# Kernel optimization log

Hardware: AMD Instinct MI355X
Metric: run time of the kernel (lower is better)

Reference implementation:

```python
import jax, jax.numpy as jnp
import numpy as np

LN_EPS = 1e-5
DIM = 128
HEADS = 6
DIM_HEAD = 32
INNER = HEADS * DIM_HEAD          # 192
FF_INNER = int(DIM * 4 * 2 / 3)   # 341 (GEGLU inner dim)
LOCAL_WINDOW = 200
CACHE = 3
COMPRESS = 2
TW = LOCAL_WINDOW + CACHE         # 203
B = 2
T = 12800                         # 32 chunks of 400


def layer_norm(x, w, b):
    m = x.mean(-1, keepdims=True)
    v = ((x - m) ** 2).mean(-1, keepdims=True)
    return (x - m) / jnp.sqrt(v + LN_EPS) * w + b


def apply_rotary(q, k):
    # q, k: (b, h, n, d); standard half-rotation rotary over absolute positions
    d = q.shape[-1]
    n = q.shape[2]
    inv_freq = 1.0 / (10000.0 ** (jnp.arange(0, d, 2, dtype=jnp.float32) / d))
    freqs = jnp.arange(n, dtype=jnp.float32)[:, None] * inv_freq  # (n, d/2)
    emb = jnp.concatenate([freqs, freqs], axis=-1)                # (n, d)
    cos = jnp.cos(emb).astype(q.dtype)
    sin = jnp.sin(emb).astype(q.dtype)

    def rot_half(x):
        x1, x2 = jnp.split(x, 2, axis=-1)
        return jnp.concatenate([-x2, x1], axis=-1)

    rope = lambda x: x * cos + rot_half(x) * sin
    return rope(q), rope(k)


def local_attention(q, k, v, w):
    # causal local attention, look_backward=1 window, look_forward=0 (lucidrains LocalAttention)
    b, h, n, d = q.shape
    nw = n // w
    q, k = apply_rotary(q, k)
    qw = q.reshape(b, h, nw, w, d)

    def look_around(x):
        xw = x.reshape(b, h, nw, w, d)
        prev = jnp.pad(xw[:, :, :-1], ((0, 0), (0, 0), (1, 0), (0, 0), (0, 0)))
        return jnp.concatenate([prev, xw], axis=3)  # (b,h,nw,2w,d)

    kw = look_around(k)
    vw = look_around(v)

    t = jnp.arange(n).reshape(nw, w)
    tk_prev = jnp.pad(t[:-1], ((1, 0), (0, 0)), constant_values=-1)
    tk = jnp.concatenate([tk_prev, t], axis=1)  # (nw, 2w); -1 marks padding
    mask = (t[:, :, None] >= tk[:, None, :]) & (tk[:, None, :] >= 0)  # (nw, w, 2w)

    sim = jnp.einsum('bhwid,bhwjd->bhwij', qw, kw) * (d ** -0.5)
    neg = jnp.finfo(sim.dtype).min
    sim = jnp.where(mask[None, None], sim, neg)
    attn = jax.nn.softmax(sim, axis=-1)
    out = jnp.einsum('bhwij,bhwjd->bhwid', attn, vw)
    return out.reshape(b, h, n, d)


def local_mha(x, ln_w, ln_b, wqkv, wo, window):
    h = layer_norm(x, ln_w, ln_b)
    qkv = h @ wqkv                       # (b, n, 3*INNER)
    q, k, v = jnp.split(qkv, 3, axis=-1)

    def split_heads(t):
        bb, n, _ = t.shape
        return t.reshape(bb, n, HEADS, DIM_HEAD).transpose(0, 2, 1, 3)

    out = local_attention(split_heads(q), split_heads(k), split_heads(v), window)
    bb, hh, n, d = out.shape
    out = out.transpose(0, 2, 1, 3).reshape(bb, n, hh * d)
    return out @ wo


def feed_forward(x, ln_w, ln_b, w1, w2):
    h = layer_norm(x, ln_w, ln_b) @ w1   # (b, n, 2*FF_INNER)
    a, gate = jnp.split(h, 2, axis=-1)
    return (a * jax.nn.gelu(gate, approximate=False)) @ w2


def local_trans(x, ln1_w, ln1_b, wqkv, wo, ln2_w, ln2_b, w1, w2, window):
    n_layers = ln1_w.shape[0]
    for i in range(n_layers):
        x = x + local_mha(x, ln1_w[i], ln1_b[i], wqkv[i], wo[i], window)
        x = x + feed_forward(x, ln2_w[i], ln2_b[i], w1[i], w2[i])
    return x


def setup_inputs() -> dict:
    key = jax.random.key(0)
    ks = jax.random.split(key, 16)
    std = 0.02
    rn = lambda k, shape: jax.random.normal(k, shape, dtype=jnp.float32) * std
    inp = {
        'x': jax.random.normal(ks[0], (B, DIM, T), dtype=jnp.float32),
        'cache_token': jax.random.normal(ks[1], (1, CACHE * COMPRESS, DIM), dtype=jnp.float32),
    }
    ki = 2
    for g in ('dt', 'lt'):
        inp[g + '_ln1_w'] = jnp.ones((2, DIM), jnp.float32)
        inp[g + '_ln1_b'] = jnp.zeros((2, DIM), jnp.float32)
        inp[g + '_wqkv'] = rn(ks[ki], (2, DIM, 3 * INNER)); ki += 1
        inp[g + '_wo'] = rn(ks[ki], (2, INNER, DIM)); ki += 1
        inp[g + '_ln2_w'] = jnp.ones((2, DIM), jnp.float32)
        inp[g + '_ln2_b'] = jnp.zeros((2, DIM), jnp.float32)
        inp[g + '_w1'] = rn(ks[ki], (2, DIM, 2 * FF_INNER)); ki += 1
        inp[g + '_w2'] = rn(ks[ki], (2, FF_INNER, DIM)); ki += 1
    inp['conv_w'] = rn(ks[ki], (DIM, DIM, COMPRESS)); ki += 1
    inp['conv_b'] = jnp.zeros((DIM,), jnp.float32)
    return inp


def reference(x, cache_token,
              dt_ln1_w, dt_ln1_b, dt_wqkv, dt_wo, dt_ln2_w, dt_ln2_b, dt_w1, dt_w2,
              lt_ln1_w, lt_ln1_b, lt_wqkv, lt_wo, lt_ln2_w, lt_ln2_b, lt_w1, lt_w2,
              conv_w, conv_b):
    feat = x.transpose(0, 2, 1)                     # (B, T, C)
    b, t, c = feat.shape
    chunk = LOCAL_WINDOW * COMPRESS                 # 400
    nchunks = t // chunk
    feat = feat.reshape(b, nchunks, chunk, c)
    ct = jnp.broadcast_to(cache_token[:, None], (b, nchunks, CACHE * COMPRESS, c))
    feat = jnp.concatenate([ct, feat], axis=2)      # interleave cache tokens per chunk
    feat = feat.reshape(b, nchunks * (chunk + CACHE * COMPRESS), c)

    # DownTrans: 2-layer local transformer (window 406) + strided conv compress
    feat = local_trans(feat, dt_ln1_w, dt_ln1_b, dt_wqkv, dt_wo,
                       dt_ln2_w, dt_ln2_b, dt_w1, dt_w2, TW * COMPRESS)
    y = jax.lax.conv_general_dilated(
        feat.transpose(0, 2, 1), conv_w, (COMPRESS,), 'VALID',
        dimension_numbers=('NCH', 'OIH', 'NCH')) + conv_b[None, :, None]
    feat = y.transpose(0, 2, 1)                     # (B, n/2, C)

    # remaining depth-2 local transformer (window 203)
    feat = local_trans(feat, lt_ln1_w, lt_ln1_b, lt_wqkv, lt_wo,
                       lt_ln2_w, lt_ln2_b, lt_w1, lt_w2, TW)
    return feat
```

## Files before the change

### kernel.cpp

```cpp
#include <hip/hip_runtime.h>
#include <cstdint>
#include <cstddef>

#define DIM    128
#define HEADS  6
#define INNER  192
#define QKV3   576
#define FFI    341
#define FF2    682
#define GGP    352
#define BATCH  2
#define T_IN   12800
#define N1     12992
#define N2     6496
#define ROWS1  (BATCH * N1)
#define ROWS2  (BATCH * N2)
#define W_DT   406
#define W_LT   203

typedef unsigned short ushortT;
typedef unsigned int u32;
typedef __bf16 bf16x8 __attribute__((ext_vector_type(8)));
typedef float f32x4 __attribute__((ext_vector_type(4)));

__device__ __forceinline__ f32x4 mfma16(bf16x8 a, bf16x8 b, f32x4 c) {
  return __builtin_amdgcn_mfma_f32_16x16x32_bf16(a, b, c, 0, 0, 0);
}
__device__ __forceinline__ ushortT f2bf(float x) {
  union { __bf16 b; ushortT u; } c; c.b = (__bf16)x; return c.u;
}
__device__ __forceinline__ void async_copy16(const ushortT* g, ushortT* l) {
  __builtin_amdgcn_global_load_lds(
      (const __attribute__((address_space(1))) unsigned int*)g,
      (__attribute__((address_space(3))) unsigned int*)l, 16, 0, 0);
}

static constexpr size_t OF_FEAT = 0;
static constexpr size_t OF_H    = OF_FEAT + (size_t)ROWS1 * DIM;
static constexpr size_t OF_QKH  = OF_H + (size_t)ROWS1 * DIM / 2;
static constexpr size_t SZ_QKH  = ((size_t)(ROWS1 + 128) * 384) / 2;
static constexpr size_t OF_AO   = OF_QKH + SZ_QKH;
static constexpr size_t OF_VT   = OF_AO + (size_t)ROWS1 * INNER / 2;
static constexpr size_t SZ_VT   = ((size_t)384 * (N1 + 128)) / 2;
static constexpr size_t OF_GG   = OF_VT + SZ_VT;
static constexpr size_t OF_F2   = OF_GG + (size_t)ROWS1 * GGP / 2;
static constexpr size_t OF_WT   = OF_F2 + (size_t)ROWS2 * DIM;
static constexpr size_t WT_QKV = 0;
static constexpr size_t WT_WO  = 81920;
static constexpr size_t WT_W1  = 106496;
static constexpr size_t WT_W2  = 204800;
static constexpr size_t WT_SET = 249856;
static constexpr size_t OF_CW  = OF_WT + (4 * WT_SET) / 2 + 64;
static constexpr size_t OF_ROPE = OF_CW + (128 * 256) / 2 + 64;
static constexpr size_t OF_H2  = OF_ROPE + (size_t)N1 * 32;

__global__ void build_feat_kernel(const float* __restrict__ x,
                                  const float* __restrict__ cache,
                                  float* __restrict__ feat) {
  int idx = blockIdx.x * 256 + threadIdx.x;
  if (idx >= ROWS1 * DIM) return;
  int d = idx & 127;
  int row = idx >> 7;
  int b = row / N1;
  int i = row - b * N1;
  int c = i / 406;
  int j = i - c * 406;
  float v;
  if (j < 6) v = cache[j * DIM + d];
  else       v = x[((size_t)b * DIM + d) * T_IN + (c * 400 + j - 6)];
  feat[idx] = v;
}

__global__ __launch_bounds__(256) void ln_kernel(const float* __restrict__ x,
                                                 ushortT* __restrict__ y,
                                                 const float* __restrict__ w,
                                                 const float* __restrict__ bb,
                                                 int rows) {
  int row = blockIdx.x * 4 + (threadIdx.x >> 6);
  if (row >= rows) return;
  int lane = threadIdx.x & 63;
  const float* xr = x + (size_t)row * DIM;
  float2 v = *(const float2*)(xr + lane * 2);
  float s = v.x + v.y;
#pragma unroll
  for (int off = 32; off; off >>= 1) s += __shfl_xor(s, off);
  float mean = s * (1.0f / 128.0f);
  float dx = v.x - mean, dy = v.y - mean;
  float q = dx * dx + dy * dy;
#pragma unroll
  for (int off = 32; off; off >>= 1) q += __shfl_xor(q, off);
  float rstd = rsqrtf(q * (1.0f / 128.0f) + 1e-5f);
  float2 wv = *(const float2*)(w + lane * 2);
  float2 bv = *(const float2*)(bb + lane * 2);
  u32 packed = (u32)f2bf(dx * rstd * wv.x + bv.x) |
               ((u32)f2bf(dy * rstd * wv.y + bv.y) << 16);
  *(u32*)(y + (size_t)row * DIM + lane * 2) = packed;
}

__global__ __launch_bounds__(256) void gemm_nln(
    const ushortT* __restrict__ A, int lda,
    const ushortT* __restrict__ Wt, int ldw,
    const float* __restrict__ C, float* __restrict__ Co,
    const float* __restrict__ bias,
    int M, int Kpad, int addC,
    const float* __restrict__ lnw, const float* __restrict__ lnb,
    ushortT* __restrict__ hout, ushortT* __restrict__ bfout) {
  __shared__ ushortT As[2][64 * 32];
  __shared__ ushortT Bs[2][128 * 32];
  __shared__ float lnS[64][4];
  const int tid = threadIdx.x;
  const int wid = tid >> 6, lane = tid & 63;
  const int ck = lane & 15, quad = lane >> 4;
  const int bm = blockIdx.y * 64;
  const int wr = (wid >> 1) * 32, wc = (wid & 1) * 64;
  const int half = wid & 1;
  f32x4 acc[2][4];
#pragma unroll
  for (int t = 0; t < 2; t++)
#pragma unroll
    for (int u = 0; u < 4; u++) acc[t][u] = (f32x4){0.f, 0.f, 0.f, 0.f};

  auto stage = [&](int bsel, int k0) {
    {
      int idx = wid * 64 + lane;
      int row = idx >> 2, seg = (idx & 3) << 3;
      async_copy16(A + (size_t)(bm + row) * lda + k0 + seg,
                   As[bsel] + (size_t)(wid * 64) * 8);
    }
#pragma unroll
    for (int c2 = 0; c2 < 2; c2++) {
      int idx = c2 * 256 + wid * 64 + lane;
      int row = idx >> 2, seg = (idx & 3) << 3;
      async_copy16(Wt + (size_t)row * ldw + k0 + seg,
                   Bs[bsel] + (size_t)(c2 * 256 + wid * 64) * 8);
    }
  };

  stage(0, 0);
  __syncthreads();
  const int nt = Kpad >> 5;
  for (int t = 0; t < nt; t++) {
    const int cur = t & 1;
    if (t + 1 < nt) stage(cur ^ 1, (t + 1) << 5);
    bf16x8 af[2], bfr[4];
#pragma unroll
    for (int tt = 0; tt < 2; tt++)
      af[tt] = *(const bf16x8*)&As[cur][(wr + tt * 16 + ck) * 32 + quad * 8];
#pragma unroll
    for (int u = 0; u < 4; u++)
      bfr[u] = *(const bf16x8*)&Bs[cur][(wc + u * 16 + ck) * 32 + quad * 8];
#pragma unroll
    for (int tt = 0; tt < 2; tt++)
#pragma unroll
      for (int u = 0; u < 4; u++)
        acc[tt][u] = mfma16(af[tt], bfr[u], acc[tt][u]);
    __syncthreads();
  }

  float bv4[4] = {0.f, 0.f, 0.f, 0.f};
  if (bias) {
#pragma unroll
    for (int u = 0; u < 4; u++) bv4[u] = bias[wc + u * 16 + ck];
  }
  float res[2][4][4];
#pragma unroll
  for (int t = 0; t < 2; t++) {
#pragma unroll
    for (int r = 0; r < 4; r++) {
      int row = bm + wr + t * 16 + quad * 4 + r;
      const float* crow = C + (size_t)row * DIM;
#pragma unroll
      for (int u = 0; u < 4; u++) {
        int col = wc + u * 16 + ck;
        float v = acc[t][u][r] + bv4[u];
        if (addC) v += crow[col];
        res[t][r][u] = v;
      }
      if (Co) {
        float* orow = Co + (size_t)row * DIM;
#pragma unroll
        for (int u = 0; u < 4; u++) orow[wc + u * 16 + ck] = res[t][r][u];
      }
      if (bfout) {
        ushortT* brow = bfout + (size_t)row * DIM;
#pragma unroll
        for (int u = 0; u < 4; u++) brow[wc + u * 16 + ck] = f2bf(res[t][r][u]);
      }
    }
  }

  if (hout) {
#pragma unroll
    for (int t = 0; t < 2; t++) {
#pragma unroll
      for (int r = 0; r < 4; r++) {
        float s1 = ((res[t][r][0] + res[t][r][1]) + (res[t][r][2] + res[t][r][3]));
        float s2 = ((res[t][r][0] * res[t][r][0] + res[t][r][1] * res[t][r][1]) +
                    (res[t][r][2] * res[t][r][2] + res[t][r][3] * res[t][r][3]));
        s1 += __shfl_xor(s1, 1); s2 += __shfl_xor(s2, 1);
        s1 += __shfl_xor(s1, 2); s2 += __shfl_xor(s2, 2);
        s1 += __shfl_xor(s1, 4); s2 += __shfl_xor(s2, 4);
        s1 += __shfl_xor(s1, 8); s2 += __shfl_xor(s2, 8);
        if (ck == 0) {
          int rowIn = wr + t * 16 + quad * 4 + r;
          lnS[rowIn][half * 2]     = s1;
          lnS[rowIn][half * 2 + 1] = s2;
        }
      }
    }
    __syncthreads();
    float lw[4], lb[4];
#pragma unroll
    for (int u = 0; u < 4; u++) {
      lw[u] = lnw[wc + u * 16 + ck];
      lb[u] = lnb[wc + u * 16 + ck];
    }
#pragma unroll
    for (int t = 0; t < 2; t++) {
#pragma unroll
      for (int r = 0; r < 4; r++) {
        int rowIn = wr + t * 16 + quad * 4 + r;
        float S1 = lnS[rowIn][0] + lnS[rowIn][2];
        float S2 = lnS[rowIn][1] + lnS[rowIn][3];
        float mean = S1 * (1.0f / 128.0f);
        float var = S2 * (1.0f / 128.0f) - mean * mean;
        float rstd = rsqrtf(var + 1e-5f);
        ushortT* hrow = hout + (size_t)(bm + rowIn) * DIM;
#pragma unroll
        for (int u = 0; u < 4; u++) {
          int col = wc + u * 16 + ck;
          hrow[col] = f2bf((res[t][r][u] - mean) * rstd * lw[u] + lb[u]);
        }
      }
    }
  }
}

__global__ __launch_bounds__(256) void gemm_qkv(
    const ushortT* __restrict__ A,
    const ushortT* __restrict__ Wt,
    const float2* __restrict__ rope,
    ushortT* __restrict__ qkh,
    ushortT* __restrict__ vt,
    int M, int nseq, int nseqP) {
  __shared__ ushortT As[2][128 * 32];
  __shared__ ushortT Bs[2][128 * 32];
  const int tid = threadIdx.x;
  const int wid = tid >> 6, lane = tid & 63;
  const int ck = lane & 15, quad = lane >> 4;
  const int bm = blockIdx.y * 128, bn = blockIdx.x * 128;
  const int wr = (wid >> 1) * 64, wc = (wid & 1) * 64;
  f32x4 acc[4][4];
#pragma unroll
  for (int t = 0; t < 4; t++)
#pragma unroll
    for (int u = 0; u < 4; u++) acc[t][u] = (f32x4){0.f, 0.f, 0.f, 0.f};

  auto stage = [&](int bsel, int k0) {
#pragma unroll
    for (int c2 = 0; c2 < 2; c2++) {
      int idx = c2 * 256 + wid * 64 + lane;
      int row = idx >> 2, seg = (idx & 3) << 3;
      int ar = bm + row; if (ar > M - 1) ar = M - 1;
      async_copy16(A + (size_t)ar * 128 + k0 + seg,
                   As[bsel] + (size_t)(c2 * 256 + wid * 64) * 8);
      async_copy16(Wt + (size_t)(bn + row) * 128 + k0 + seg,
                   Bs[bsel] + (size_t)(c2 * 256 + wid * 64) * 8);
    }
  };

  stage(0, 0);
  __syncthreads();
  for (int t = 0; t < 4; t++) {
    const int cur = t & 1;
    if (t < 3) stage(cur ^ 1, (t + 1) * 32);
    bf16x8 af[4], bfr[4];
#pragma unroll
    for (int tt = 0; tt < 4; tt++)
      af[tt] = *(const bf16x8*)&As[cur][(wr + tt * 16 + ck) * 32 + quad * 8];
#pragma unroll
    for (int u = 0; u < 4; u++)
      bfr[u] = *(const bf16x8*)&Bs[cur][(wc + u * 16 + ck) * 32 + quad * 8];
#pragma unroll
    for (int tt = 0; tt < 4; tt++)
#pragma unroll
      for (int u = 0; u < 4; u++)
        acc[tt][u] = mfma16(af[tt], bfr[u], acc[tt][u]);
    __syncthreads();
  }

  const int s = bn + wc;
  if (s >= QKV3) return;

  if (s < 384) {
    const bool isQ = s < 192;
    const float SCq = 0.17677669529663687f * 1.4426950408889634f;
#pragma unroll
    for (int t = 0; t < 4; t++) {
#pragma unroll
      for (int r = 0; r < 4; r++) {
        int row = bm + wr + t * 16 + quad * 4 + r;
        if (row >= M) continue;
        int pos = (row >= nseq) ? row - nseq : row;
        float2 cssn = rope[pos * 16 + ck];
        float cs = cssn.x, sn = cssn.y;
        ushortT* orow = qkh + (size_t)row * 384;
#pragma unroll
        for (int u = 0; u < 4; u += 2) {
          float a0 = acc[t][u][r], a1 = acc[t][u + 1][r];
          float o0 = a0 * cs - a1 * sn;
          float o1 = a1 * cs + a0 * sn;
          if (isQ) { o0 *= SCq; o1 *= SCq; }
          int c0 = s + u * 16 + ck;
          orow[c0]      = f2bf(o0);
          orow[c0 + 16] = f2bf(o1);
        }
      }
    }
  } else {
#pragma unroll
    for (int t = 0; t < 4; t++) {
      int rowb = bm + wr + t * 16 + quad * 4;
      if (rowb >= M) continue;
      int bb = (rowb >= nseq) ? 1 : 0;
      int posb = rowb - bb * nseq;
#pragma unroll
      for (int u = 0; u < 4; u++) {
        int cv = s - 384 + u * 16 + ck;
        int hh = cv >> 5, d = cv & 31;
        ushort4 o;
        o.x = f2bf(acc[t][u][0]);
        o.y = f2bf(acc[t][u][1]);
        o.z = f2bf(acc[t][u][2]);
        o.w = f2bf(acc[t][u][3]);
        *(ushort4*)(vt + ((size_t)((bb * 6 + hh) * 32 + d)) * nseqP + posb) = o;
      }
    }
  }
}

__global__ __launch_bounds__(256) void gemm_w1g(
    const ushortT* __restrict__ A,
    const ushortT* __restrict__ Wt,
    ushortT* __restrict__ gg,
    int M) {
  __shared__ ushortT As[2][128 * 32];
  __shared__ ushortT Bs[2][128 * 32];
  const int tid = threadIdx.x;
  const int wid = tid >> 6, lane = tid & 63;
  const int ck = lane & 15, quad = lane >> 4;
  const int bm = blockIdx.y * 128, bn = blockIdx.x * 128;
  const int wr = (wid >> 1) * 64, wc = (wid & 1) * 64;
  f32x4 acc[4][4];
#pragma unroll
  for (int t = 0; t < 4; t++)
#pragma unroll
    for (int u = 0; u < 4; u++) acc[t][u] = (f32x4){0.f, 0.f, 0.f, 0.f};

  auto stage = [&](int bsel, int k0) {
#pragma unroll
    for (int c2 = 0; c2 < 2; c2++) {
      int idx = c2 * 256 + wid * 64 + lane;
      int row = idx >> 2, seg = (idx & 3) << 3;
      int ar = bm + row; if (ar > M - 1) ar = M - 1;
      async_copy16(A + (size_t)ar * 128 + k0 + seg,
                   As[bsel] + (size_t)(c2 * 256 + wid * 64) * 8);
      async_copy16(Wt + (size_t)(bn + row) * 128 + k0 + seg,
                   Bs[bsel] + (size_t)(c2 * 256 + wid * 64) * 8);
    }
  };

  stage(0, 0);
  __syncthreads();
  for (int t = 0; t < 4; t++) {
    const int cur = t & 1;
    if (t < 3) stage(cur ^ 1, (t + 1) * 32);
    bf16x8 af[4], bfr[4];
#pragma unroll
    for (int tt = 0; tt < 4; tt++)
      af[tt] = *(const bf16x8*)&As[cur][(wr + tt * 16 + ck) * 32 + quad * 8];
#pragma unroll
    for (int u = 0; u < 4; u++)
      bfr[u] = *(const bf16x8*)&Bs[cur][(wc + u * 16 + ck) * 32 + quad * 8];
#pragma unroll
    for (int tt = 0; tt < 4; tt++)
#pragma unroll
      for (int u = 0; u < 4; u++)
        acc[tt][u] = mfma16(af[tt], bfr[u], acc[tt][u]);
    __syncthreads();
  }

  const int s = bn + wc;
  if (s >= 704) return;
#pragma unroll
  for (int t = 0; t < 4; t++) {
#pragma unroll
    for (int r = 0; r < 4; r++) {
      int row = bm + wr + t * 16 + quad * 4 + r;
      if (row >= M) continue;
      ushortT* orow = gg + (size_t)row * GGP;
#pragma unroll
      for (int u = 0; u < 4; u += 2) {
        float a  = acc[t][u][r];
        float gt = acc[t][u + 1][r];
        float ge = 0.5f * gt * (1.0f + erff(gt * 0.70710678118654752f));
        int p = ((s + u * 16) >> 5) * 16 + ck;
        orow[p] = f2bf(a * ge);
      }
    }
  }
}

__global__ __launch_bounds__(256) void attn_kernel(
    const ushortT* __restrict__ qkh, const ushortT* __restrict__ vt,
    ushortT* __restrict__ out, int nseq, int nseqP, int w, int nw, int qgroups) {
  __shared__ __align__(16) ushortT Ks[2][64 * 32];
  __shared__ __align__(16) ushortT Vs[2][32 * 64];

  const int bx = blockIdx.x;
  const int c = bx % nw;
  const int g = (qgroups - 1) - bx / nw;
  const int h = blockIdx.y;
  const int b = blockIdx.z;
  const int tid = threadIdx.x;
  const int wv = tid >> 6;
  const int lane = tid & 63;
  const int ck = lane & 15;
  const int quad = lane >> 4;

  const ushortT* gq = qkh + (size_t)b * nseq * 384;
  const ushortT* gv = vt + ((size_t)(b * 6 + h) * 32) * nseqP;
  const int cw = c * w;
  const int q0 = g * 64;
  const int qt = q0 + wv * 16;
  const bool wave_on = qt < w;

  const int j0 = (c > 0) ? (c - 1) * w : 0;
  const int jend_block = cw + min(q0 + 63, w - 1) + 1;
  const int jend_wave = wave_on ? (cw + min(qt + 15, w - 1) + 1) : 0;
  const int ntiles = (jend_block - j0 + 63) >> 6;

  bf16x8 qf;
  {
    int qrow = cw + min(qt + ck, w - 1);
    qf = *(const bf16x8*)(gq + (size_t)qrow * 384 + h * 32 + quad * 8);
  }

  const int krow = tid >> 2, kch = tid & 3;
  const int krho = ((krow >> 5) << 5) | (((krow >> 2) & 1) << 4) |
                   (((krow >> 3) & 3) << 2) | (krow & 3);
  const int kslot = krho * 4 + kch;
  const int kphys = kslot ^ ((kslot >> 3) & 7);
  const ushortT* ksrc = gq + (size_t)krow * 384 + 192 + h * 32 + kch * 8;
  const int vphys = tid ^ ((tid >> 3) & 7);
  const ushortT* vsrc = gv + (size_t)(tid >> 3) * nseqP + (tid & 7) * 8;

  const int kbase = ((4 * ck + quad) ^ (ck >> 1)) * 8;
  const int p0 = ((8 * ck + quad) ^ (ck & 7)) * 8;
  const int p1 = p0 ^ 32;

  f32x4 olo = {0.f, 0.f, 0.f, 0.f};
  f32x4 ohi = {0.f, 0.f, 0.f, 0.f};
  f32x4 accl = {0.f, 0.f, 0.f, 0.f};
  bf16x8 onesf;
  {
    union { u32 u[4]; bf16x8 v; } o_;
    o_.u[0] = o_.u[1] = o_.u[2] = o_.u[3] = 0x3F803F80u;
    onesf = o_.v;
  }

  auto tileoff = [&](int t) -> int { return j0 + 64 * min(t, ntiles - 1); };

  float4 kX, vX, kY, vY;
  {
    float4 k0 = *(const float4*)(ksrc + (size_t)j0 * 384);
    float4 v0 = *(const float4*)(vsrc + j0);
    *(float4*)&Ks[0][(size_t)kphys * 8] = k0;
    *(float4*)&Vs[0][(size_t)vphys * 8] = v0;
    kX = *(const float4*)(ksrc + (size_t)tileoff(1) * 384);
    vX = *(const float4*)(vsrc + tileoff(1));
    kY = *(const float4*)(ksrc + (size_t)tileoff(2) * 384);
    vY = *(const float4*)(vsrc + tileoff(2));
  }

  auto compute = [&](const ushortT* KsB, const ushortT* VsB, int tb) {
    if (tb >= jend_wave) return;
    bf16x8 kf0 = *(const bf16x8*)&KsB[kbase];
    bf16x8 kf1 = *(const bf16x8*)&KsB[kbase + 512];
    bf16x8 kf2 = *(const bf16x8*)&KsB[kbase + 1024];
    bf16x8 kf3 = *(const bf16x8*)&KsB[kbase + 1536];
    bf16x8 vlo0 = *(const bf16x8*)&VsB[p0];
    bf16x8 vlo1 = *(const bf16x8*)&VsB[p1];
    bf16x8 vhi0 = *(const bf16x8*)&VsB[p0 + 1024];
    bf16x8 vhi1 = *(const bf16x8*)&VsB[p1 + 1024];
    f32x4 z = {0.f, 0.f, 0.f, 0.f};
    f32x4 s0 = mfma16(kf0, qf, z);
    f32x4 s1 = mfma16(kf1, qf, z);
    f32x4 s2 = mfma16(kf2, qf, z);
    f32x4 s3 = mfma16(kf3, qf, z);
    if (tb + 63 > cw + qt) {
      int q = cw + qt + ck;
      int kb = tb + 8 * quad;
#pragma unroll
      for (int r = 0; r < 4; r++) {
        if (kb + r > q)      s0[r] = -__builtin_inff();
        if (kb + 4 + r > q)  s1[r] = -__builtin_inff();
        if (kb + 32 + r > q) s2[r] = -__builtin_inff();
        if (kb + 36 + r > q) s3[r] = -__builtin_inff();
      }
    }
    float e00 = exp2f(s0[0]), e01 = exp2f(s0[1]), e02 = exp2f(s0[2]), e03 = exp2f(s0[3]);
    float e10 = exp2f(s1[0]), e11 = exp2f(s1[1]), e12 = exp2f(s1[2]), e13 = exp2f(s1[3]);
    float e20 = exp2f(s2[0]), e21 = exp2f(s2[1]), e22 = exp2f(s2[2]), e23 = exp2f(s2[3]);
    float e30 = exp2f(s3[0]), e31 = exp2f(s3[1]), e32 = exp2f(s3[2]), e33 = exp2f(s3[3]);
    union { bf16x8 v; u32 u[4]; } pa0, pa1;
    pa0.u[0] = (u32)f2bf(e00) | ((u32)f2bf(e01) << 16);
    pa0.u[1] = (u32)f2bf(e02) | ((u32)f2bf(e03) << 16);
    pa0.u[2] = (u32)f2bf(e10) | ((u32)f2bf(e11) << 16);
    pa0.u[3] = (u32)f2bf(e12) | ((u32)f2bf(e13) << 16);
    pa1.u[0] = (u32)f2bf(e20) | ((u32)f2bf(e21) << 16);
    pa1.u[1] = (u32)f2bf(e22) | ((u32)f2bf(e23) << 16);
    pa1.u[2] = (u32)f2bf(e30) | ((u32)f2bf(e31) << 16);
    pa1.u[3] = (u32)f2bf(e32) | ((u32)f2bf(e33) << 16);
    olo  = mfma16(pa0.v, vlo0, olo);
    olo  = mfma16(pa1.v, vlo1, olo);
    ohi  = mfma16(pa0.v, vhi0, ohi);
    ohi  = mfma16(pa1.v, vhi1, ohi);
    accl = mfma16(pa0.v, onesf, accl);
    accl = mfma16(pa1.v, onesf, accl);
  };

  for (int i = 0; i < ntiles; i += 2) {
    __syncthreads();
    *(float4*)&Ks[1][(size_t)kphys * 8] = kX;
    *(float4*)&Vs[1][(size_t)vphys * 8] = vX;
    kX = *(const float4*)(ksrc + (size_t)tileoff(i + 3) * 384);
    vX = *(const float4*)(vsrc + tileoff(i + 3));
    compute(Ks[0], Vs[0], j0 + i * 64);

    __syncthreads();
    *(float4*)&Ks[0][(size_t)kphys * 8] = kY;
    *(float4*)&Vs[0][(size_t)vphys * 8] = vY;
    kY = *(const float4*)(ksrc + (size_t)tileoff(i + 4) * 384);
    vY = *(const float4*)(vsrc + tileoff(i + 4));
    compute(Ks[1], Vs[1], j0 + (i + 1) * 64);
  }

  if (wave_on) {
#pragma unroll
    for (int r = 0; r < 4; r++) {
      int qi = qt + quad * 4 + r;
      if (qi < w) {
        float invr = 1.0f / accl[r];
        ushortT* orow = out + ((size_t)b * nseq + cw + qi) * INNER + h * 32;
        orow[ck]      = f2bf(olo[r] * invr);
        orow[ck + 16] = f2bf(ohi[r] * invr);
      }
    }
  }
}

__global__ void wconvert_all_kernel(
    const float* __restrict__ dq, const float* __restrict__ dwo,
    const float* __restrict__ dw1, const float* __restrict__ dw2,
    const float* __restrict__ lq, const float* __restrict__ lwo,
    const float* __restrict__ lw1, const float* __restrict__ lw2,
    const float* __restrict__ convw,
    ushortT* __restrict__ wt, ushortT* __restrict__ cwt,
    float2* __restrict__ rope) {
  int idx = blockIdx.x * 256 + threadIdx.x;
  const int TOTW = 4 * (int)WT_SET;
  const int CWN = 128 * 256;
  if (idx < TOTW) {
    int s = idx / (int)WT_SET;
    int rem = idx - s * (int)WT_SET;
    int lyr = s & 1;
    const float* Wq = ((s < 2) ? dq : lq) + (size_t)lyr * DIM * QKV3;
    const float* Wo = ((s < 2) ? dwo : lwo) + (size_t)lyr * INNER * DIM;
    const float* W1 = ((s < 2) ? dw1 : lw1) + (size_t)lyr * DIM * FF2;
    const float* W2 = ((s < 2) ? dw2 : lw2) + (size_t)lyr * FFI * DIM;
    float v = 0.f;
    if (rem < (int)WT_WO) {
      int n = rem >> 7, k = rem & 127;
      if (n < QKV3) v = Wq[(size_t)k * QKV3 + n];
    } else if (rem < (int)WT_W1) {
      int r = rem - (int)WT_WO;
      int n = r / INNER, k = r - n * INNER;
      v = Wo[(size_t)k * DIM + n];
    } else if (rem < (int)WT_W2) {
      int r = rem - (int)WT_W1;
      int n = r >> 7, k = r & 127;
      if (n < 704) {
        int blk = n >> 5, wi = n & 31;
        int p = blk * 16 + (wi & 15);
        if (p < FFI) {
          int src = (wi < 16) ? p : FFI + p;
          v = W1[(size_t)k * FF2 + src];
        }
      }
    } else {
      int r = rem - (int)WT_W2;
      int n = r / GGP, k = r - n * GGP;
      if (k < FFI) v = W2[(size_t)k * DIM + n];
    }
    wt[idx] = f2bf(v);
  } else if (idx < TOTW + CWN) {
    int r = idx - TOTW;
    int o = r >> 8, k = r & 255;
    int kk = k >> 7, i = k & 127;
    cwt[r] = f2bf(convw[((size_t)o * DIM + i) * 2 + kk]);
  } else {
    int r = idx - TOTW - CWN;
    if (r < N1 * 16) {
      int pos = r >> 4, k = r & 15;
      float invf = 1.0f / powf(10000.0f, (float)k * (1.0f / 16.0f));
      float sn, cs;
      sincosf((float)pos * invf, &sn, &cs);
      rope[r] = make_float2(cs, sn);
    }
  }
}

static void run_layer(float* F, float* Fout, ushortT* hbuf, ushortT* qkh, ushortT* vtb,
                      ushortT* attnb, ushortT* ggb, const ushortT* wt,
                      const float2* rope,
                      int M, int nseq, int w,
                      const float* ln2w, const float* ln2b,
                      const float* nlnw, const float* nlnb,
                      ushortT* w2bf, hipStream_t stream) {
  int nseqP = nseq + 128;
  int gy = (M + 127) / 128;
  int gy64 = M / 64;
  gemm_qkv<<<dim3(5, gy), 256, 0, stream>>>(hbuf, wt + WT_QKV, rope, qkh, vtb, M, nseq, nseqP);
  int nw = nseq / w;
  int qgroups = (w + 63) / 64;
  attn_kernel<<<dim3(nw * qgroups, HEADS, BATCH), 256, 0, stream>>>(qkh, vtb, attnb,
                                                                    nseq, nseqP, w, nw, qgroups);
  gemm_nln<<<dim3(1, gy64), 256, 0, stream>>>(attnb, INNER, wt + WT_WO, INNER, F, F,
                                              nullptr, M, INNER, 1, ln2w, ln2b,
                                              hbuf, nullptr);
  gemm_w1g<<<dim3(6, gy), 256, 0, stream>>>(hbuf, wt + WT_W1, ggb, M);
  gemm_nln<<<dim3(1, gy64), 256, 0, stream>>>(ggb, GGP, wt + WT_W2, GGP, F, Fout,
                                              nullptr, M, GGP, 1, nlnw, nlnb,
                                              nlnw ? hbuf : (ushortT*)nullptr, w2bf);
}

extern "C" void kernel_launch(void* const* d_in, const int* in_sizes, int n_in,
                              void* d_out, int out_size, void* d_ws, size_t ws_size,
                              hipStream_t stream) {
  const float* x        = (const float*)d_in[0];
  const float* cache    = (const float*)d_in[1];
  const float* dt_ln1_w = (const float*)d_in[2];
  const float* dt_ln1_b = (const float*)d_in[3];
  const float* dt_wqkv  = (const float*)d_in[4];
  const float* dt_wo    = (const float*)d_in[5];
  const float* dt_ln2_w = (const float*)d_in[6];
  const float* dt_ln2_b = (const float*)d_in[7];
  const float* dt_w1    = (const float*)d_in[8];
  const float* dt_w2    = (const float*)d_in[9];
  const float* lt_ln1_w = (const float*)d_in[10];
  const float* lt_ln1_b = (const float*)d_in[11];
  const float* lt_wqkv  = (const float*)d_in[12];
  const float* lt_wo    = (const float*)d_in[13];
  const float* lt_ln2_w = (const float*)d_in[14];
  const float* lt_ln2_b = (const float*)d_in[15];
  const float* lt_w1    = (const float*)d_in[16];
  const float* lt_w2    = (const float*)d_in[17];
  const float* conv_w   = (const float*)d_in[18];
  const float* conv_b   = (const float*)d_in[19];

  float* ws     = (float*)d_ws;
  float* feat   = ws + OF_FEAT;
  ushortT* h    = (ushortT*)(ws + OF_H);
  ushortT* qkh  = (ushortT*)(ws + OF_QKH);
  ushortT* attnb= (ushortT*)(ws + OF_AO);
  ushortT* vtb  = (ushortT*)(ws + OF_VT);
  ushortT* ggb  = (ushortT*)(ws + OF_GG);
  float* feat2  = ws + OF_F2;
  ushortT* wt   = (ushortT*)(ws + OF_WT);
  ushortT* cwt  = (ushortT*)(ws + OF_CW);
  float2* rope  = (float2*)(ws + OF_ROPE);
  ushortT* h2   = (ushortT*)(ws + OF_H2);
  float* outf   = (float*)d_out;

  {
    int total = 4 * (int)WT_SET + 128 * 256 + N1 * 16;
    wconvert_all_kernel<<<(total + 255) / 256, 256, 0, stream>>>(
        dt_wqkv, dt_wo, dt_w1, dt_w2, lt_wqkv, lt_wo, lt_w1, lt_w2,
        conv_w, wt, cwt, rope);
  }

  build_feat_kernel<<<(ROWS1 * DIM + 255) / 256, 256, 0, stream>>>(x, cache, feat);
  ln_kernel<<<ROWS1 / 4, 256, 0, stream>>>(feat, h, dt_ln1_w, dt_ln1_b, ROWS1);

  run_layer(feat, feat, h, qkh, vtb, attnb, ggb, wt + 0 * WT_SET, rope,
            ROWS1, N1, W_DT,
            dt_ln2_w, dt_ln2_b, dt_ln1_w + DIM, dt_ln1_b + DIM, nullptr, stream);
  run_layer(feat, nullptr, h, qkh, vtb, attnb, ggb, wt + 1 * WT_SET, rope,
            ROWS1, N1, W_DT,
            dt_ln2_w + DIM, dt_ln2_b + DIM, nullptr, nullptr, h, stream);

  gemm_nln<<<dim3(1, ROWS2 / 64), 256, 0, stream>>>(h, 256, cwt, 256,
                                                    feat2, feat2, conv_b,
                                                    ROWS2, 256, 0,
                                                    lt_ln1_w, lt_ln1_b, h2, nullptr);

  run_layer(feat2, feat2, h2, qkh, vtb, attnb, ggb, wt + 2 * WT_SET, rope,
            ROWS2, N2, W_LT,
            lt_ln2_w, lt_ln2_b, lt_ln1_w + DIM, lt_ln1_b + DIM, nullptr, stream);
  run_layer(feat2, outf, h2, qkh, vtb, attnb, ggb, wt + 3 * WT_SET, rope,
            ROWS2, N2, W_LT,
            lt_ln2_w + DIM, lt_ln2_b + DIM, nullptr, nullptr, nullptr, stream);
}
```

Before: 542.2 us.

## Triple-buffer QKV/W1 GEMM staging and use non-draining barriers in attention

```diff
diff --git a/kernel.cpp b/kernel.cpp
--- a/kernel.cpp
+++ b/kernel.cpp
@@ -33,6 +33,11 @@
   __builtin_amdgcn_global_load_lds(
       (const __attribute__((address_space(1))) unsigned int*)g,
       (__attribute__((address_space(3))) unsigned int*)l, 16, 0, 0);
+}
+__device__ __forceinline__ void bar_nodrain() {
+  asm volatile("s_waitcnt lgkmcnt(0)" ::: "memory");
+  __builtin_amdgcn_s_barrier();
+  __builtin_amdgcn_sched_barrier(0);
 }
 
 static constexpr size_t OF_FEAT = 0;
@@ -243,8 +248,8 @@
     ushortT* __restrict__ qkh,
     ushortT* __restrict__ vt,
     int M, int nseq, int nseqP) {
-  __shared__ ushortT As[2][128 * 32];
-  __shared__ ushortT Bs[2][128 * 32];
+  __shared__ ushortT As[3][128 * 32];
+  __shared__ ushortT Bs[3][128 * 32];
   const int tid = threadIdx.x;
   const int wid = tid >> 6, lane = tid & 63;
   const int ck = lane & 15, quad = lane >> 4;
@@ -270,10 +275,16 @@
   };
 
   stage(0, 0);
-  __syncthreads();
+  stage(1, 32);
+#pragma unroll
   for (int t = 0; t < 4; t++) {
-    const int cur = t & 1;
-    if (t < 3) stage(cur ^ 1, (t + 1) * 32);
+    const int cur = t % 3;
+    if (t < 3) asm volatile("s_waitcnt vmcnt(4)" ::: "memory");
+    else       asm volatile("s_waitcnt vmcnt(0)" ::: "memory");
+    asm volatile("s_waitcnt lgkmcnt(0)" ::: "memory");
+    __builtin_amdgcn_s_barrier();
+    __builtin_amdgcn_sched_barrier(0);
+    if (t < 2) stage((t + 2) % 3, (t + 2) * 32);
     bf16x8 af[4], bfr[4];
 #pragma unroll
     for (int tt = 0; tt < 4; tt++)
@@ -286,7 +297,6 @@
 #pragma unroll
       for (int u = 0; u < 4; u++)
         acc[tt][u] = mfma16(af[tt], bfr[u], acc[tt][u]);
-    __syncthreads();
   }
 
   const int s = bn + wc;
@@ -344,8 +354,8 @@
     const ushortT* __restrict__ Wt,
     ushortT* __restrict__ gg,
     int M) {
-  __shared__ ushortT As[2][128 * 32];
-  __shared__ ushortT Bs[2][128 * 32];
+  __shared__ ushortT As[3][128 * 32];
+  __shared__ ushortT Bs[3][128 * 32];
   const int tid = threadIdx.x;
   const int wid = tid >> 6, lane = tid & 63;
   const int ck = lane & 15, quad = lane >> 4;
@@ -371,10 +381,16 @@
   };
 
   stage(0, 0);
-  __syncthreads();
+  stage(1, 32);
+#pragma unroll
   for (int t = 0; t < 4; t++) {
-    const int cur = t & 1;
-    if (t < 3) stage(cur ^ 1, (t + 1) * 32);
+    const int cur = t % 3;
+    if (t < 3) asm volatile("s_waitcnt vmcnt(4)" ::: "memory");
+    else       asm volatile("s_waitcnt vmcnt(0)" ::: "memory");
+    asm volatile("s_waitcnt lgkmcnt(0)" ::: "memory");
+    __builtin_amdgcn_s_barrier();
+    __builtin_amdgcn_sched_barrier(0);
+    if (t < 2) stage((t + 2) % 3, (t + 2) * 32);
     bf16x8 af[4], bfr[4];
 #pragma unroll
     for (int tt = 0; tt < 4; tt++)
@@ -387,7 +403,6 @@
 #pragma unroll
       for (int u = 0; u < 4; u++)
         acc[tt][u] = mfma16(af[tt], bfr[u], acc[tt][u]);
-    __syncthreads();
   }
 
   const int s = bn + wc;
@@ -531,14 +546,14 @@
   };
 
   for (int i = 0; i < ntiles; i += 2) {
-    __syncthreads();
+    bar_nodrain();
     *(float4*)&Ks[1][(size_t)kphys * 8] = kX;
     *(float4*)&Vs[1][(size_t)vphys * 8] = vX;
     kX = *(const float4*)(ksrc + (size_t)tileoff(i + 3) * 384);
     vX = *(const float4*)(vsrc + tileoff(i + 3));
     compute(Ks[0], Vs[0], j0 + i * 64);
 
-    __syncthreads();
+    bar_nodrain();
     *(float4*)&Ks[0][(size_t)kphys * 8] = kY;
     *(float4*)&Vs[0][(size_t)vphys * 8] = vY;
     kY = *(const float4*)(ksrc + (size_t)tileoff(i + 4) * 384);
```

Result: no change. 545.9 us (+0.7%).

## Specialize attention waves into producer loaders and consumer compute waves

Applied to the files above, without the earlier changes.

```diff
diff --git a/kernel.cpp b/kernel.cpp
--- a/kernel.cpp
+++ b/kernel.cpp
@@ -432,36 +432,54 @@
   const ushortT* gv = vt + ((size_t)(b * 6 + h) * 32) * nseqP;
   const int cw = c * w;
   const int q0 = g * 64;
-  const int qt = q0 + wv * 16;
-  const bool wave_on = qt < w;
-
   const int j0 = (c > 0) ? (c - 1) * w : 0;
   const int jend_block = cw + min(q0 + 63, w - 1) + 1;
-  const int jend_wave = wave_on ? (cw + min(qt + 15, w - 1) + 1) : 0;
   const int ntiles = (jend_block - j0 + 63) >> 6;
 
-  bf16x8 qf;
-  {
-    int qrow = cw + min(qt + ck, w - 1);
-    qf = *(const bf16x8*)(gq + (size_t)qrow * 384 + h * 32 + quad * 8);
-  }
-
-  const int krow = tid >> 2, kch = tid & 3;
-  const int krho = ((krow >> 5) << 5) | (((krow >> 2) & 1) << 4) |
-                   (((krow >> 3) & 3) << 2) | (krow & 3);
-  const int kslot = krho * 4 + kch;
-  const int kphys = kslot ^ ((kslot >> 3) & 7);
-  const ushortT* ksrc = gq + (size_t)krow * 384 + 192 + h * 32 + kch * 8;
-  const int vphys = tid ^ ((tid >> 3) & 7);
-  const ushortT* vsrc = gv + (size_t)(tid >> 3) * nseqP + (tid & 7) * 8;
+  const bool isCons = wv < 2;
+
+  const int qtA = q0 + wv * 16;
+  const int qtB = q0 + 32 + wv * 16;
+  const bool fA = isCons && (qtA < w);
+  const bool fB = isCons && (qtB < w);
+  const int jfA = fA ? (cw + min(qtA + 15, w - 1) + 1) : 0;
+  const int jfB = fB ? (cw + min(qtB + 15, w - 1) + 1) : 0;
+  const int jmaxW = max(jfA, jfB);
+
+  bf16x8 qfA, qfB;
+  if (isCons) {
+    int rA = cw + min(qtA + ck, w - 1);
+    qfA = *(const bf16x8*)(gq + (size_t)rA * 384 + h * 32 + quad * 8);
+    int rB = cw + min(qtB + ck, w - 1);
+    qfB = *(const bf16x8*)(gq + (size_t)rB * 384 + h * 32 + quad * 8);
+  }
 
   const int kbase = ((4 * ck + quad) ^ (ck >> 1)) * 8;
   const int p0 = ((8 * ck + quad) ^ (ck & 7)) * 8;
   const int p1 = p0 ^ 32;
 
-  f32x4 olo = {0.f, 0.f, 0.f, 0.f};
-  f32x4 ohi = {0.f, 0.f, 0.f, 0.f};
-  f32x4 accl = {0.f, 0.f, 0.f, 0.f};
+  const int pt = tid & 127;
+  int kphys0 = 0, kphys1 = 0, vphys0 = 0, vphys1 = 0;
+  const ushortT *ksrc0 = nullptr, *ksrc1 = nullptr, *vsrc0 = nullptr, *vsrc1 = nullptr;
+  if (!isCons) {
+#pragma unroll
+    for (int sI = 0; sI < 2; sI++) {
+      int s = pt + sI * 128;
+      int krow = s >> 2, kch = s & 3;
+      int krho = ((krow >> 5) << 5) | (((krow >> 2) & 1) << 4) |
+                 (((krow >> 3) & 3) << 2) | (krow & 3);
+      int kslot = krho * 4 + kch;
+      int kp = kslot ^ ((kslot >> 3) & 7);
+      const ushortT* ks = gq + (size_t)krow * 384 + 192 + h * 32 + kch * 8;
+      int vp = s ^ ((s >> 3) & 7);
+      const ushortT* vs = gv + (size_t)(s >> 3) * nseqP + (s & 7) * 8;
+      if (sI == 0) { kphys0 = kp; ksrc0 = ks; vphys0 = vp; vsrc0 = vs; }
+      else         { kphys1 = kp; ksrc1 = ks; vphys1 = vp; vsrc1 = vs; }
+    }
+  }
+
+  f32x4 oloA = {0.f, 0.f, 0.f, 0.f}, ohiA = {0.f, 0.f, 0.f, 0.f}, acclA = {0.f, 0.f, 0.f, 0.f};
+  f32x4 oloB = {0.f, 0.f, 0.f, 0.f}, ohiB = {0.f, 0.f, 0.f, 0.f}, acclB = {0.f, 0.f, 0.f, 0.f};
   bf16x8 onesf;
   {
     union { u32 u[4]; bf16x8 v; } o_;
@@ -471,28 +489,31 @@
 
   auto tileoff = [&](int t) -> int { return j0 + 64 * min(t, ntiles - 1); };
 
-  float4 kX, vX, kY, vY;
-  {
-    float4 k0 = *(const float4*)(ksrc + (size_t)j0 * 384);
-    float4 v0 = *(const float4*)(vsrc + j0);
-    *(float4*)&Ks[0][(size_t)kphys * 8] = k0;
-    *(float4*)&Vs[0][(size_t)vphys * 8] = v0;
-    kX = *(const float4*)(ksrc + (size_t)tileoff(1) * 384);
-    vX = *(const float4*)(vsrc + tileoff(1));
-    kY = *(const float4*)(ksrc + (size_t)tileoff(2) * 384);
-    vY = *(const float4*)(vsrc + tileoff(2));
-  }
-
-  auto compute = [&](const ushortT* KsB, const ushortT* VsB, int tb) {
-    if (tb >= jend_wave) return;
-    bf16x8 kf0 = *(const bf16x8*)&KsB[kbase];
-    bf16x8 kf1 = *(const bf16x8*)&KsB[kbase + 512];
-    bf16x8 kf2 = *(const bf16x8*)&KsB[kbase + 1024];
-    bf16x8 kf3 = *(const bf16x8*)&KsB[kbase + 1536];
-    bf16x8 vlo0 = *(const bf16x8*)&VsB[p0];
-    bf16x8 vlo1 = *(const bf16x8*)&VsB[p1];
-    bf16x8 vhi0 = *(const bf16x8*)&VsB[p0 + 1024];
-    bf16x8 vhi1 = *(const bf16x8*)&VsB[p1 + 1024];
+  float4 kX0, kX1, vX0, vX1, kY0, kY1, vY0, vY1;
+  if (!isCons) {
+    float4 a0 = *(const float4*)(ksrc0 + (size_t)j0 * 384);
+    float4 a1 = *(const float4*)(ksrc1 + (size_t)j0 * 384);
+    float4 b0 = *(const float4*)(vsrc0 + j0);
+    float4 b1 = *(const float4*)(vsrc1 + j0);
+    *(float4*)&Ks[0][(size_t)kphys0 * 8] = a0;
+    *(float4*)&Ks[0][(size_t)kphys1 * 8] = a1;
+    *(float4*)&Vs[0][(size_t)vphys0 * 8] = b0;
+    *(float4*)&Vs[0][(size_t)vphys1 * 8] = b1;
+    int t1 = tileoff(1), t2 = tileoff(2);
+    kX0 = *(const float4*)(ksrc0 + (size_t)t1 * 384);
+    kX1 = *(const float4*)(ksrc1 + (size_t)t1 * 384);
+    vX0 = *(const float4*)(vsrc0 + t1);
+    vX1 = *(const float4*)(vsrc1 + t1);
+    kY0 = *(const float4*)(ksrc0 + (size_t)t2 * 384);
+    kY1 = *(const float4*)(ksrc1 + (size_t)t2 * 384);
+    vY0 = *(const float4*)(vsrc0 + t2);
+    vY1 = *(const float4*)(vsrc1 + t2);
+  }
+
+  auto frag = [&](int tb, const bf16x8& qf, int qt,
+                  const bf16x8& kf0, const bf16x8& kf1, const bf16x8& kf2, const bf16x8& kf3,
+                  const bf16x8& vlo0, const bf16x8& vlo1, const bf16x8& vhi0, const bf16x8& vhi1,
+                  f32x4& olo, f32x4& ohi, f32x4& accl) {
     f32x4 z = {0.f, 0.f, 0.f, 0.f};
     f32x4 s0 = mfma16(kf0, qf, z);
     f32x4 s1 = mfma16(kf1, qf, z);
@@ -530,31 +551,75 @@
     accl = mfma16(pa1.v, onesf, accl);
   };
 
+  auto compute2 = [&](const ushortT* KsB, const ushortT* VsB, int tb) {
+    if (tb >= jmaxW) return;
+    bf16x8 kf0 = *(const bf16x8*)&KsB[kbase];
+    bf16x8 kf1 = *(const bf16x8*)&KsB[kbase + 512];
+    bf16x8 kf2 = *(const bf16x8*)&KsB[kbase + 1024];
+    bf16x8 kf3 = *(const bf16x8*)&KsB[kbase + 1536];
+    bf16x8 vlo0 = *(const bf16x8*)&VsB[p0];
+    bf16x8 vlo1 = *(const bf16x8*)&VsB[p1];
+    bf16x8 vhi0 = *(const bf16x8*)&VsB[p0 + 1024];
+    bf16x8 vhi1 = *(const bf16x8*)&VsB[p1 + 1024];
+    if (tb < jfA)
+      frag(tb, qfA, qtA, kf0, kf1, kf2, kf3, vlo0, vlo1, vhi0, vhi1, oloA, ohiA, acclA);
+    if (tb < jfB)
+      frag(tb, qfB, qtB, kf0, kf1, kf2, kf3, vlo0, vlo1, vhi0, vhi1, oloB, ohiB, acclB);
+  };
+
   for (int i = 0; i < ntiles; i += 2) {
     __syncthreads();
-    *(float4*)&Ks[1][(size_t)kphys * 8] = kX;
-    *(float4*)&Vs[1][(size_t)vphys * 8] = vX;
-    kX = *(const float4*)(ksrc + (size_t)tileoff(i + 3) * 384);
-    vX = *(const float4*)(vsrc + tileoff(i + 3));
-    compute(Ks[0], Vs[0], j0 + i * 64);
+    if (!isCons) {
+      *(float4*)&Ks[1][(size_t)kphys0 * 8] = kX0;
+      *(float4*)&Ks[1][(size_t)kphys1 * 8] = kX1;
+      *(float4*)&Vs[1][(size_t)vphys0 * 8] = vX0;
+      *(float4*)&Vs[1][(size_t)vphys1 * 8] = vX1;
+      int tn = tileoff(i + 3);
+      kX0 = *(const float4*)(ksrc0 + (size_t)tn * 384);
+      kX1 = *(const float4*)(ksrc1 + (size_t)tn * 384);
+      vX0 = *(const float4*)(vsrc0 + tn);
+      vX1 = *(const float4*)(vsrc1 + tn);
+    } else {
+      compute2(Ks[0], Vs[0], j0 + i * 64);
+    }
 
     __syncthreads();
-    *(float4*)&Ks[0][(size_t)kphys * 8] = kY;
-    *(float4*)&Vs[0][(size_t)vphys * 8] = vY;
-    kY = *(const float4*)(ksrc + (size_t)tileoff(i + 4) * 384);
-    vY = *(const float4*)(vsrc + tileoff(i + 4));
-    compute(Ks[1], Vs[1], j0 + (i + 1) * 64);
-  }
-
-  if (wave_on) {
+    if (!isCons) {
+      *(float4*)&Ks[0][(size_t)kphys0 * 8] = kY0;
+      *(float4*)&Ks[0][(size_t)kphys1 * 8] = kY1;
+      *(float4*)&Vs[0][(size_t)vphys0 * 8] = vY0;
+      *(float4*)&Vs[0][(size_t)vphys1 * 8] = vY1;
+      int tn = tileoff(i + 4);
+      kY0 = *(const float4*)(ksrc0 + (size_t)tn * 384);
+      kY1 = *(const float4*)(ksrc1 + (size_t)tn * 384);
+      vY0 = *(const float4*)(vsrc0 + tn);
+      vY1 = *(const float4*)(vsrc1 + tn);
+    } else {
+      compute2(Ks[1], Vs[1], j0 + (i + 1) * 64);
+    }
+  }
+
+  if (fA) {
 #pragma unroll
     for (int r = 0; r < 4; r++) {
-      int qi = qt + quad * 4 + r;
+      int qi = qtA + quad * 4 + r;
       if (qi < w) {
-        float invr = 1.0f / accl[r];
+        float invr = 1.0f / acclA[r];
         ushortT* orow = out + ((size_t)b * nseq + cw + qi) * INNER + h * 32;
-        orow[ck]      = f2bf(olo[r] * invr);
-        orow[ck + 16] = f2bf(ohi[r] * invr);
+        orow[ck]      = f2bf(oloA[r] * invr);
+        orow[ck + 16] = f2bf(ohiA[r] * invr);
+      }
+    }
+  }
+  if (fB) {
+#pragma unroll
+    for (int r = 0; r < 4; r++) {
+      int qi = qtB + quad * 4 + r;
+      if (qi < w) {
+        float invr = 1.0f / acclB[r];
+        ushortT* orow = out + ((size_t)b * nseq + cw + qi) * INNER + h * 32;
+        orow[ck]      = f2bf(oloB[r] * invr);
+        orow[ck + 16] = f2bf(ohiB[r] * invr);
       }
     }
   }
```

Measured after the change: 641.1 us. 18.2% more time.
